# Kernel tuning notes

Measured on AMD Instinct MI355X. Metric: run time of the kernel, lower is better.

## Reference

```python
import jax, jax.numpy as jnp
import numpy as np

# near_sym_b (13,19)-tap biorthogonal level-1 DTCWT filters (Kingsbury)
H0O = np.array([-0.0017578125, 0.0, 0.022265625, -0.046875, -0.0482421875,
                0.296875, 0.5554687500, 0.296875, -0.0482421875, -0.046875,
                0.022265625, 0.0, -0.0017578125], dtype=np.float32)
H1O = np.array([-7.0626e-05, 0.0, 1.34189e-03, -1.88341e-03, -7.15660e-03,
                2.38560e-02, 5.56431e-02, -5.16881e-02, -2.99758e-01,
                5.59431e-01, -2.99758e-01, -5.16881e-02, 5.56431e-02,
                2.38560e-02, -7.15660e-03, -1.88341e-03, 1.34189e-03,
                0.0, -7.0626e-05], dtype=np.float32)

def _alt(h):
    c = (len(h) - 1) // 2
    return (h * ((-1.0) ** (np.arange(len(h)) - c))).astype(np.float32)

G0O = _alt(H1O)  # synthesis lowpass  (PR complement of H1O)
G1O = _alt(H0O)  # synthesis highpass (PR complement of H0O)

DIM, HS, WS, BATCH, NB, BS = 64, 56, 56, 32, 4, 16


def _filt(x, h, axis):
    # depthwise 1D correlation with symmetric padding; x: (B,C,H,W), axis in {2,3}
    L = len(h); p = L // 2
    pad = [(0, 0)] * 4; pad[axis] = (p, p)
    xp = jnp.pad(x, pad, mode='symmetric')
    k = jnp.asarray(h, x.dtype).reshape((1, 1, L, 1) if axis == 2 else (1, 1, 1, L))
    B, C = x.shape[:2]
    y = jax.lax.conv_general_dilated(
        xp.reshape((B * C, 1) + xp.shape[2:]), k, (1, 1), 'VALID',
        dimension_numbers=('NCHW', 'OIHW', 'NCHW'))
    return y.reshape((B, C) + y.shape[2:])


def _q2c(y):
    y = y * np.float32(1.0 / np.sqrt(2.0))
    a = y[..., 0::2, 0::2]; b = y[..., 0::2, 1::2]
    c = y[..., 1::2, 0::2]; d = y[..., 1::2, 1::2]
    return (a - d, b + c), (a + d, b - c)


def _c2q(w1r, w1i, w2r, w2i):
    sc = np.float32(1.0 / np.sqrt(2.0))
    B, C, Hh, Wh = w1r.shape
    top = jnp.stack([(w1r + w2r) * sc, (w1i + w2i) * sc], axis=-1).reshape(B, C, Hh, 2 * Wh)
    bot = jnp.stack([(w1i - w2i) * sc, (w2r - w1r) * sc], axis=-1).reshape(B, C, Hh, 2 * Wh)
    return jnp.stack([top, bot], axis=3).reshape(B, C, 2 * Hh, 2 * Wh)


def dtcwt_fwd_j1(x):
    lo = _filt(x, H0O, 3); hi = _filt(x, H1O, 3)
    ll = _filt(lo, H0O, 2)
    (d15r, d15i), (d165r, d165i) = _q2c(_filt(lo, H1O, 2))   # LH -> 15/165 deg
    (d75r, d75i), (d105r, d105i) = _q2c(_filt(hi, H0O, 2))   # HL -> 75/105 deg
    (d45r, d45i), (d135r, d135i) = _q2c(_filt(hi, H1O, 2))   # HH -> 45/135 deg
    real = jnp.stack([d15r, d45r, d75r, d105r, d135r, d165r], axis=2)
    imag = jnp.stack([d15i, d45i, d75i, d105i, d135i, d165i], axis=2)
    return ll, jnp.stack([real, imag], axis=-1)  # (B,C,H,W), (B,C,6,H/2,W/2,2)


def dtcwt_inv_j1(ll, yh):
    r = yh[..., 0]; im = yh[..., 1]
    lh = _c2q(r[:, :, 0], im[:, :, 0], r[:, :, 5], im[:, :, 5])
    hl = _c2q(r[:, :, 2], im[:, :, 2], r[:, :, 3], im[:, :, 3])
    hh = _c2q(r[:, :, 1], im[:, :, 1], r[:, :, 4], im[:, :, 4])
    lo = _filt(ll, G0O, 2) + _filt(lh, G1O, 2)
    hi = _filt(hl, G0O, 2) + _filt(hh, G1O, 2)
    return _filt(lo, G0O, 3) + _filt(hi, G1O, 3)


def setup_inputs():
    key = jax.random.key(0)
    ks = jax.random.split(key, 6)
    return {
        'x': jax.random.normal(ks[0], (BATCH, HS * WS, DIM), jnp.float32),
        'w_ll': jax.random.normal(ks[1], (DIM, HS, WS), jnp.float32) * 0.02,
        'w1': jax.random.normal(ks[2], (2, NB, BS, BS), jnp.float32) * 0.02,
        'w2': jax.random.normal(ks[3], (2, NB, BS, BS), jnp.float32) * 0.02,
        'b1': jax.random.normal(ks[4], (2, NB, BS), jnp.float32) * 0.02,
        'b2': jax.random.normal(ks[5], (2, NB, BS), jnp.float32) * 0.02,
        'H': HS, 'W': WS,
    }


def reference(x, w_ll, w1, w2, b1, b2, H, W):
    Bt, N, C = x.shape
    xi = jnp.transpose(x.reshape(Bt, H, W, C), (0, 3, 1, 2)).astype(jnp.float32)
    xl, xh = dtcwt_fwd_j1(xi)
    xl = xl * w_ll                                  # (B,C,H,W) * (C,H,W)
    Hh, Wh = H // 2, W // 2
    # (B,C,6,Hh,Wh,2) -> (2,B,6,Hh,Wh,C) -> split C into (NB,BS) blocks
    xh = jnp.transpose(xh, (5, 0, 2, 3, 4, 1)).reshape(2, Bt, 6, Hh, Wh, NB, BS)
    xr, xim = xh[0], xh[1]
    mul = lambda t, w: jnp.einsum('...bd,bdk->...bk', t, w)
    r1 = jax.nn.relu(mul(xr, w1[0]) - mul(xim, w1[1]) + b1[0])
    i1 = jax.nn.relu(mul(xr, w1[1]) + mul(xim, w1[0]) + b1[1])
    r2 = mul(r1, w2[0]) - mul(i1, w2[1]) + b2[0]
    i2 = mul(r1, w2[1]) + mul(i1, w2[0]) + b2[1]
    xh2 = jnp.stack([r2, i2], axis=-1).reshape(Bt, 6, Hh, Wh, C, 2)
    xh2 = jnp.transpose(xh2, (0, 4, 1, 2, 3, 5))    # (B,C,6,Hh,Wh,2)
    y = dtcwt_inv_j1(xl, xh2)
    return jnp.transpose(y, (0, 2, 3, 1)).reshape(Bt, N, C)
```

## Files before the change

kernel.cpp:

```cpp
#include <hip/hip_runtime.h>

#define BT 32
#define CH 64
#define HS 56
#define WS 56
#define HH 28
#define WH 28

namespace {
constexpr float ISQ2 = 0.70710678118654752440f;
constexpr float F_H0[13] = {-0.0017578125f, 0.0f, 0.022265625f, -0.046875f,
    -0.0482421875f, 0.296875f, 0.55546875f, 0.296875f, -0.0482421875f,
    -0.046875f, 0.022265625f, 0.0f, -0.0017578125f};
constexpr float F_H1[19] = {-7.0626e-05f, 0.0f, 0.00134189f, -0.00188341f,
    -0.0071566f, 0.023856f, 0.0556431f, -0.0516881f, -0.299758f, 0.559431f,
    -0.299758f, -0.0516881f, 0.0556431f, 0.023856f, -0.0071566f,
    -0.00188341f, 0.00134189f, 0.0f, -7.0626e-05f};
constexpr float F_G0[19] = {7.0626e-05f, 0.0f, -0.00134189f, -0.00188341f,
    0.0071566f, 0.023856f, -0.0556431f, -0.0516881f, 0.299758f, 0.559431f,
    0.299758f, -0.0516881f, -0.0556431f, 0.023856f, 0.0071566f,
    -0.00188341f, -0.00134189f, 0.0f, 7.0626e-05f};
constexpr float F_G1[13] = {-0.0017578125f, 0.0f, 0.022265625f, 0.046875f,
    -0.0482421875f, -0.296875f, 0.55546875f, -0.296875f, -0.0482421875f,
    0.046875f, 0.022265625f, 0.0f, -0.0017578125f};
}

__device__ __forceinline__ int symi(int k) {
    k = (k < 0) ? (-1 - k) : k;
    k = (k >= HS) ? (2 * HS - 1 - k) : k;
    return k;
}

__device__ __forceinline__ unsigned short f2bf(float f) {
    unsigned u = __float_as_uint(f);
    u += 0x7fffu + ((u >> 16) & 1u);
    return (unsigned short)(u >> 16);
}
__device__ __forceinline__ float bf2f(unsigned short h) {
    return __uint_as_float(((unsigned)h) << 16);
}
__device__ __forceinline__ float2 bfp2(unsigned u) {
    float2 r;
    r.x = __uint_as_float((u & 0xffffu) << 16);
    r.y = __uint_as_float(u & 0xffff0000u);
    return r;
}
__device__ __forceinline__ unsigned packbf(float a, float b) {
    return (unsigned)f2bf(a) | ((unsigned)f2bf(b) << 16);
}

typedef __attribute__((ext_vector_type(8))) short short8;
typedef __attribute__((ext_vector_type(4))) float f32x4;

#define PPOS 784

__global__ __launch_bounds__(256) void k_wll_T(const float* __restrict__ wll,
                                               float* __restrict__ wllT) {
    __shared__ float tile[64][65];
    int pos0 = blockIdx.x * 64;
    int lp = threadIdx.x & 63, g = threadIdx.x >> 6;
#pragma unroll
    for (int r = 0; r < 16; ++r) {
        int cc = r * 4 + g;
        tile[cc][lp] = wll[cc * (HS * WS) + pos0 + lp];
    }
    __syncthreads();
#pragma unroll
    for (int r = 0; r < 16; ++r) {
        int pl = r * 4 + g;
        wllT[(pos0 + pl) * CH + lp] = tile[lp][pl];
    }
}

__global__ __launch_bounds__(256) void k_fwd_rows(const float* __restrict__ x,
                                                  unsigned short* __restrict__ lo,
                                                  unsigned short* __restrict__ hi) {
    int b = blockIdx.x / HS, h = blockIdx.x % HS;
    int strip = threadIdx.x >> 5;
    int c0 = (threadIdx.x & 31) * 2;
    int base = (b * HS + h) * WS * CH + c0;
    const float* row = x + base;
    unsigned short* lop = lo + base;
    unsigned short* hip = hi + base;
    int w0s = strip * 7;
    float Wa[19], Wb[19];
#pragma unroll
    for (int t = 0; t < 19; ++t) {
        float2 v = *(const float2*)(row + symi(w0s - 9 + t) * CH);
        Wa[t] = v.x; Wb[t] = v.y;
    }
    float2 nW[7];
#pragma unroll
    for (int u = 0; u < 7; ++u) nW[u] = *(const float2*)(row + symi(w0s + u + 10) * CH);
#pragma unroll
    for (int u = 0; u < 7; ++u) {
        int w = w0s + u;
        float aLo = 0.f, aHi = 0.f, bLo = 0.f, bHi = 0.f;
#pragma unroll
        for (int t = 0; t < 13; ++t) { aLo += F_H0[t] * Wa[3 + t]; bLo += F_H0[t] * Wb[3 + t]; }
#pragma unroll
        for (int t = 0; t < 19; ++t) { aHi += F_H1[t] * Wa[t]; bHi += F_H1[t] * Wb[t]; }
        *(unsigned*)(lop + w * CH) = packbf(aLo, bLo);
        *(unsigned*)(hip + w * CH) = packbf(aHi, bHi);
#pragma unroll
        for (int t = 0; t < 18; ++t) { Wa[t] = Wa[t + 1]; Wb[t] = Wb[t + 1]; }
        Wa[18] = nW[u].x; Wb[18] = nW[u].y;
    }
}

__global__ __launch_bounds__(256) void k_cols_lo(
    const unsigned short* __restrict__ lo, const float* __restrict__ wllT,
    float* __restrict__ xl, unsigned short* __restrict__ sbT) {
    __shared__ float qT[4][64][15];
    int hf = blockIdx.y;
    int b = blockIdx.x / WH, wp = blockIdx.x % WH;
    int w0 = 2 * wp, tid = threadIdx.x;
    int q = tid >> 6, c = tid & 63;
    int rp = q >> 1, jc = q & 1;
    const unsigned short* colbase = lo + (b * HS) * WS * CH + (w0 + jc) * CH + c;
    {
        int hstart = 2 * (hf * 14) + rp;
        float W[19];
#pragma unroll
        for (int t = 0; t < 19; ++t) W[t] = bf2f(colbase[symi(hstart - 9 + t) * (WS * CH)]);
        for (int g = 0; g < 2; ++g) {
            float nW0[7], nW1[7], nwll[7];
            int ii0 = g * 7;
#pragma unroll
            for (int u = 0; u < 7; ++u) {
                int h = hstart + 2 * (ii0 + u);
                nW0[u] = bf2f(colbase[symi(h + 10) * (WS * CH)]);
                nW1[u] = bf2f(colbase[symi(h + 11) * (WS * CH)]);
            }
#pragma unroll
            for (int u = 0; u < 7; ++u) {
                int h = hstart + 2 * (ii0 + u);
                nwll[u] = wllT[(h * WS + (w0 + jc)) * CH + c];
            }
#pragma unroll
            for (int u = 0; u < 7; ++u) {
                int ii = ii0 + u;
                int h = hstart + 2 * ii;
                float vll = 0.f, vlh = 0.f;
#pragma unroll
                for (int t = 0; t < 13; ++t) vll += F_H0[t] * W[3 + t];
#pragma unroll
                for (int t = 0; t < 19; ++t) vlh += F_H1[t] * W[t];
                xl[((b * HS + h) * WS + (w0 + jc)) * CH + c] = vll * nwll[u];
                qT[q][c][ii] = vlh;
#pragma unroll
                for (int t = 0; t < 17; ++t) W[t] = W[t + 2];
                W[17] = nW0[u];
                W[18] = nW1[u];
            }
        }
    }
    __syncthreads();
    {
        int qq = tid >> 5;
        int role = qq & 3, half = qq >> 2;
        int c0 = (tid & 31) * 2;
        int rowA = role & 1, rowB = 3 - (role & 1);
        float sgn = (role == 1 || role == 2) ? 1.f : -1.f;
        int p = (role < 2) ? role : role + 8;
        const float* qA0 = &qT[rowA][c0][0];
        const float* qA1 = &qT[rowA][c0 + 1][0];
        const float* qB0 = &qT[rowB][c0][0];
        const float* qB1 = &qT[rowB][c0 + 1][0];
        unsigned short* dst = sbT + ((p * BT + b) * PPOS + wp * 28 + hf * 14) * CH + c0;
#pragma unroll
        for (int g = 0; g < 7; ++g) {
            int ii = half * 7 + g;
            float v0 = (qA0[ii] + sgn * qB0[ii]) * ISQ2;
            float v1 = (qA1[ii] + sgn * qB1[ii]) * ISQ2;
            *(unsigned*)(dst + ii * CH) = packbf(v0, v1);
        }
    }
}

__global__ __launch_bounds__(256) void k_cols_hi(const unsigned short* __restrict__ hi,
                                                 unsigned short* __restrict__ sbT) {
    __shared__ float qT[2][4][64][15];
    int hf = blockIdx.y;
    int b = blockIdx.x / WH, wp = blockIdx.x % WH;
    int w0 = 2 * wp, tid = threadIdx.x;
    int q = tid >> 6, c = tid & 63;
    int rp = q >> 1, jc = q & 1;
    const unsigned short* colbase = hi + (b * HS) * WS * CH + (w0 + jc) * CH + c;
    {
        int hstart = 2 * (hf * 14) + rp;
        float W[19];
#pragma unroll
        for (int t = 0; t < 19; ++t) W[t] = bf2f(colbase[symi(hstart - 9 + t) * (WS * CH)]);
        for (int g = 0; g < 2; ++g) {
            float nW0[7], nW1[7];
            int ii0 = g * 7;
#pragma unroll
            for (int u = 0; u < 7; ++u) {
                int h = hstart + 2 * (ii0 + u);
                nW0[u] = bf2f(colbase[symi(h + 10) * (WS * CH)]);
                nW1[u] = bf2f(colbase[symi(h + 11) * (WS * CH)]);
            }
#pragma unroll
            for (int u = 0; u < 7; ++u) {
                int ii = ii0 + u;
                float vhl = 0.f, vhh = 0.f;
#pragma unroll
                for (int t = 0; t < 13; ++t) vhl += F_H0[t] * W[3 + t];
#pragma unroll
                for (int t = 0; t < 19; ++t) vhh += F_H1[t] * W[t];
                qT[0][q][c][ii] = vhl;
                qT[1][q][c][ii] = vhh;
#pragma unroll
                for (int t = 0; t < 17; ++t) W[t] = W[t + 2];
                W[17] = nW0[u];
                W[18] = nW1[u];
            }
        }
    }
    __syncthreads();
    {
        int qq = tid >> 5;
        int role = qq & 3, half = qq >> 2;
        int c0 = (tid & 31) * 2;
        int rowA = role & 1, rowB = 3 - (role & 1);
        float sgn = (role == 1 || role == 2) ? 1.f : -1.f;
#pragma unroll
        for (int src = 0; src < 2; ++src) {
            int p = (src == 0) ? (4 + role) : ((role < 2) ? (2 + role) : (6 + role));
            const float* qA0 = &qT[src][rowA][c0][0];
            const float* qA1 = &qT[src][rowA][c0 + 1][0];
            const float* qB0 = &qT[src][rowB][c0][0];
            const float* qB1 = &qT[src][rowB][c0 + 1][0];
            unsigned short* dst = sbT + ((p * BT + b) * PPOS + wp * 28 + hf * 14) * CH + c0;
#pragma unroll
            for (int g = 0; g < 7; ++g) {
                int ii = half * 7 + g;
                float v0 = (qA0[ii] + sgn * qB0[ii]) * ISQ2;
                float v1 = (qA1[ii] + sgn * qB1[ii]) * ISQ2;
                *(unsigned*)(dst + ii * CH) = packbf(v0, v1);
            }
        }
    }
}

__global__ __launch_bounds__(256) void k_mix(
    const unsigned short* __restrict__ sbT, const float* __restrict__ w1,
    const float* __restrict__ w2, const float* __restrict__ b1,
    const float* __restrict__ b2, unsigned short* __restrict__ P0,
    unsigned short* __restrict__ P1, unsigned short* __restrict__ P2) {
    __shared__ unsigned short l1a[4][16][36];
    __shared__ unsigned short l1b[4][16][36];
    int blk = blockIdx.x;
    int pr = blk / (BT * 7);
    int rem = blk % (BT * 7);
    int b = rem / 7;
    int chunk = rem % 7;
    int sa = (pr == 0) ? 0 : (pr == 1) ? 2 : 1;
    int sb = (pr == 0) ? 5 : (pr == 1) ? 3 : 4;
    unsigned short* Pd = (pr == 0) ? P0 : (pr == 1) ? P1 : P2;
    int tid = threadIdx.x;
    int lane = tid & 63;
    int wv = tid >> 6;
    int nb = __builtin_amdgcn_readfirstlane(wv);
    int quad = lane >> 4;
    int n = lane & 15;

    short8 B1r, B1i, B2r, B2i;
#pragma unroll
    for (int j = 0; j < 8; ++j) {
        int kk = quad * 8 + j;
        int riw = kk >> 4, dd = kk & 15;
        float v1r = w1[nb * 256 + dd * 16 + n];
        float v1i = w1[1024 + nb * 256 + dd * 16 + n];
        float v2r = w2[nb * 256 + dd * 16 + n];
        float v2i = w2[1024 + nb * 256 + dd * 16 + n];
        B1r[j] = (short)f2bf(riw ? -v1i : v1r);
        B1i[j] = (short)f2bf(riw ? v1r : v1i);
        B2r[j] = (short)f2bf(riw ? -v2i : v2r);
        B2i[j] = (short)f2bf(riw ? v2r : v2i);
    }
    float bias1r = b1[nb * 16 + n], bias1i = b1[64 + nb * 16 + n];
    float bias2r = b2[nb * 16 + n], bias2i = b2[64 + nb * 16 + n];

    int rix = quad >> 1, dlo = (quad & 1) * 8;
    const unsigned short* pAa =
        sbT + (((sa * 2 + rix) * BT + b) * PPOS + n) * CH + nb * 16 + dlo;
    const unsigned short* pAb =
        sbT + (((sb * 2 + rix) * BT + b) * PPOS + n) * CH + nb * 16 + dlo;

    int pbase = chunk * 112;
    for (int t = 0; t < 7; ++t) {
        int pos0 = pbase + t * 16;
        short8 A1a = *(const short8*)(pAa + pos0 * CH);
        short8 A1b = *(const short8*)(pAb + pos0 * CH);
        f32x4 a1r = {bias1r, bias1r, bias1r, bias1r};
        f32x4 a1i = {bias1i, bias1i, bias1i, bias1i};
        f32x4 b1r_ = a1r, b1i_ = a1i;
        a1r = __builtin_amdgcn_mfma_f32_16x16x32_bf16(A1a, B1r, a1r, 0, 0, 0);
        a1i = __builtin_amdgcn_mfma_f32_16x16x32_bf16(A1a, B1i, a1i, 0, 0, 0);
        b1r_ = __builtin_amdgcn_mfma_f32_16x16x32_bf16(A1b, B1r, b1r_, 0, 0, 0);
        b1i_ = __builtin_amdgcn_mfma_f32_16x16x32_bf16(A1b, B1i, b1i_, 0, 0, 0);
#pragma unroll
        for (int r = 0; r < 4; ++r) {
            int pos = quad * 4 + r;
            l1a[wv][pos][n] = f2bf(fmaxf(a1r[r], 0.f));
            l1a[wv][pos][16 + n] = f2bf(fmaxf(a1i[r], 0.f));
            l1b[wv][pos][n] = f2bf(fmaxf(b1r_[r], 0.f));
            l1b[wv][pos][16 + n] = f2bf(fmaxf(b1i_[r], 0.f));
        }
        union { short8 s8; uint2 u2[2]; } a2a, a2b;
        const unsigned short* rowpa = &l1a[wv][n][0];
        const unsigned short* rowpb = &l1b[wv][n][0];
        a2a.u2[0] = *(const uint2*)(rowpa + quad * 8);
        a2a.u2[1] = *(const uint2*)(rowpa + quad * 8 + 4);
        a2b.u2[0] = *(const uint2*)(rowpb + quad * 8);
        a2b.u2[1] = *(const uint2*)(rowpb + quad * 8 + 4);
        f32x4 aAr = {bias2r, bias2r, bias2r, bias2r};
        f32x4 aAi = {bias2i, bias2i, bias2i, bias2i};
        f32x4 aBr = aAr, aBi = aAi;
        aAr = __builtin_amdgcn_mfma_f32_16x16x32_bf16(a2a.s8, B2r, aAr, 0, 0, 0);
        aAi = __builtin_amdgcn_mfma_f32_16x16x32_bf16(a2a.s8, B2i, aAi, 0, 0, 0);
        aBr = __builtin_amdgcn_mfma_f32_16x16x32_bf16(a2b.s8, B2r, aBr, 0, 0, 0);
        aBi = __builtin_amdgcn_mfma_f32_16x16x32_bf16(a2b.s8, B2i, aBi, 0, 0, 0);
#pragma unroll
        for (int r = 0; r < 4; ++r) {
            int pos_g = pos0 + quad * 4 + r;
            int wp = pos_g / 28, ii = pos_g - wp * 28;
            int o = ((b * HS + 2 * ii) * WS + 2 * wp) * CH + nb * 16 + n;
            Pd[o] = f2bf((aAr[r] + aBr[r]) * ISQ2);
            Pd[o + CH] = f2bf((aAi[r] + aBi[r]) * ISQ2);
            Pd[o + WS * CH] = f2bf((aAi[r] - aBi[r]) * ISQ2);
            Pd[o + WS * CH + CH] = f2bf((aBr[r] - aAr[r]) * ISQ2);
        }
    }
}

template <int MODE>
__device__ __forceinline__ void inv_cols_body(
    const float* __restrict__ xl, const unsigned short* __restrict__ P0,
    const unsigned short* __restrict__ P1, const unsigned short* __restrict__ P2,
    float* __restrict__ lo2, float* __restrict__ hi2) {
    int hf = blockIdx.y;
    int b = blockIdx.x / 7, wg = blockIdx.x % 7;
    int wl = threadIdx.x >> 5, l = threadIdx.x & 31;
    int c0 = l * 2;
    int w = wg * 8 + wl;
    int base = (b * HS) * WS * CH + w * CH + c0;
    const int st = WS * CH;
    const unsigned short* Bp = (MODE == 0) ? P0 : P2;
    float* outp = (MODE == 0) ? lo2 : hi2;
    auto ldA = [&](int r) -> float2 {
        if (MODE == 0) return *(const float2*)(xl + base + r * st);
        return bfp2(*(const unsigned*)(P1 + base + r * st));
    };
    auto ldB = [&](int r) -> float2 {
        return bfp2(*(const unsigned*)(Bp + base + r * st));
    };
    int h0 = hf * 28;
    float Aa[19], Ab[19], Ba[13], Bb[13];
#pragma unroll
    for (int t = 0; t < 19; ++t) { float2 v = ldA(symi(h0 - 9 + t)); Aa[t] = v.x; Ab[t] = v.y; }
#pragma unroll
    for (int t = 0; t < 13; ++t) { float2 v = ldB(symi(h0 - 6 + t)); Ba[t] = v.x; Bb[t] = v.y; }
    for (int g = 0; g < 7; ++g) {
        float2 nA[4], nB[4];
        int hg = h0 + g * 4;
#pragma unroll
        for (int u = 0; u < 4; ++u) nA[u] = ldA(symi(hg + u + 10));
#pragma unroll
        for (int u = 0; u < 4; ++u) nB[u] = ldB(symi(hg + u + 7));
#pragma unroll
        for (int u = 0; u < 4; ++u) {
            int h = hg + u;
            float acca = 0.f, accb = 0.f;
#pragma unroll
            for (int t = 0; t < 19; ++t) { acca += F_G0[t] * Aa[t]; accb += F_G0[t] * Ab[t]; }
#pragma unroll
            for (int t = 0; t < 13; ++t) { acca += F_G1[t] * Ba[t]; accb += F_G1[t] * Bb[t]; }
            float2 ov; ov.x = acca; ov.y = accb;
            *(float2*)(outp + base + h * st) = ov;
#pragma unroll
            for (int t = 0; t < 18; ++t) { Aa[t] = Aa[t + 1]; Ab[t] = Ab[t + 1]; }
#pragma unroll
            for (int t = 0; t < 12; ++t) { Ba[t] = Ba[t + 1]; Bb[t] = Bb[t + 1]; }
            Aa[18] = nA[u].x; Ab[18] = nA[u].y;
            Ba[12] = nB[u].x; Bb[12] = nB[u].y;
        }
    }
}

__global__ __launch_bounds__(256) void k_inv_cols(
    const float* __restrict__ xl, const unsigned short* __restrict__ P0,
    const unsigned short* __restrict__ P1, const unsigned short* __restrict__ P2,
    float* __restrict__ lo2, float* __restrict__ hi2) {
    if (blockIdx.z == 0)
        inv_cols_body<0>(xl, P0, P1, P2, lo2, hi2);
    else
        inv_cols_body<1>(xl, P0, P1, P2, lo2, hi2);
}

__global__ __launch_bounds__(256) void k_inv_rows(const float* __restrict__ lo2,
                                                  const float* __restrict__ hi2,
                                                  float* __restrict__ out) {
    int b = blockIdx.x / HS, h = blockIdx.x % HS;
    int strip = threadIdx.x >> 5;
    int c0 = (threadIdx.x & 31) * 2;
    int base = (b * HS + h) * WS * CH + c0;
    const float* rlo = lo2 + base;
    const float* rhi = hi2 + base;
    float* op = out + base;
    int w0s = strip * 7;
    float Aa[19], Ab[19], Ba[13], Bb[13];
#pragma unroll
    for (int t = 0; t < 19; ++t) {
        float2 v = *(const float2*)(rlo + symi(w0s - 9 + t) * CH);
        Aa[t] = v.x; Ab[t] = v.y;
    }
#pragma unroll
    for (int t = 0; t < 13; ++t) {
        float2 v = *(const float2*)(rhi + symi(w0s - 6 + t) * CH);
        Ba[t] = v.x; Bb[t] = v.y;
    }
    float2 nA[7], nB[7];
#pragma unroll
    for (int u = 0; u < 7; ++u) nA[u] = *(const float2*)(rlo + symi(w0s + u + 10) * CH);
#pragma unroll
    for (int u = 0; u < 7; ++u) nB[u] = *(const float2*)(rhi + symi(w0s + u + 7) * CH);
#pragma unroll
    for (int u = 0; u < 7; ++u) {
        int w = w0s + u;
        float acca = 0.f, accb = 0.f;
#pragma unroll
        for (int t = 0; t < 19; ++t) { acca += F_G0[t] * Aa[t]; accb += F_G0[t] * Ab[t]; }
#pragma unroll
        for (int t = 0; t < 13; ++t) { acca += F_G1[t] * Ba[t]; accb += F_G1[t] * Bb[t]; }
        float2 ov; ov.x = acca; ov.y = accb;
        *(float2*)(op + w * CH) = ov;
#pragma unroll
        for (int t = 0; t < 18; ++t) { Aa[t] = Aa[t + 1]; Ab[t] = Ab[t + 1]; }
#pragma unroll
        for (int t = 0; t < 12; ++t) { Ba[t] = Ba[t + 1]; Bb[t] = Bb[t + 1]; }
        Aa[18] = nA[u].x; Ab[18] = nA[u].y;
        Ba[12] = nB[u].x; Bb[12] = nB[u].y;
    }
}

extern "C" void kernel_launch(void* const* d_in, const int* in_sizes, int n_in,
                              void* d_out, int out_size, void* d_ws, size_t ws_size,
                              hipStream_t stream) {
    const float* x = (const float*)d_in[0];
    const float* w_ll = (const float*)d_in[1];
    const float* w1 = (const float*)d_in[2];
    const float* w2 = (const float*)d_in[3];
    const float* b1 = (const float*)d_in[4];
    const float* b2 = (const float*)d_in[5];
    float* out = (float*)d_out;

    const size_t A = (size_t)BT * HS * WS * CH;
    const size_t SBf = (size_t)12 * 64 * BT * PPOS / 2;
    float* wsf = (float*)d_ws;
    float* xl = wsf;
    unsigned short* sbT = (unsigned short*)(wsf + A);
    float* lo2 = wsf + A;
    float* hi2 = wsf + A + SBf;
    unsigned short* lo_in = (unsigned short*)(wsf + A + SBf + A);
    unsigned short* hi_in = lo_in + A;
    unsigned short* P0 = hi_in + A;
    unsigned short* P1 = P0 + A;
    unsigned short* P2 = P1 + A;

    float* wllT = out;

    k_wll_T<<<49, 256, 0, stream>>>(w_ll, wllT);
    k_fwd_rows<<<BT * HS, 256, 0, stream>>>(x, lo_in, hi_in);
    k_cols_lo<<<dim3(BT * WH, 2), 256, 0, stream>>>(lo_in, wllT, xl, sbT);
    k_cols_hi<<<dim3(BT * WH, 2), 256, 0, stream>>>(hi_in, sbT);
    k_mix<<<3 * BT * 7, 256, 0, stream>>>(sbT, w1, w2, b1, b2, P0, P1, P2);
    k_inv_cols<<<dim3(BT * 7, 2, 2), 256, 0, stream>>>(xl, P0, P1, P2, lo2, hi2);
    k_inv_rows<<<BT * HS, 256, 0, stream>>>(lo2, hi2, out);
}
```

Measured before the change: 180.1 us.

## Merge forward column kernels and split column/mix kernels into finer grids

Merges the lo and hi forward column kernels into one launch that uses a z-dimension to pick the source, and halves the rows each block handles (7 instead of 14) so the grid has more blocks. The mix kernel moves from 4 waves per block to one 64-thread block per channel group with a grid y dimension, and prefetches the next A tile in a register double buffer. The inverse column kernel also splits its height into quarters. The aim is more parallelism and one fewer launch, in exchange for more halo reloading of the filter window per block.

```diff
diff --git a/kernel.cpp b/kernel.cpp
--- a/kernel.cpp
+++ b/kernel.cpp
@@ -108,161 +108,106 @@
     }
 }
 
-__global__ __launch_bounds__(256) void k_cols_lo(
-    const unsigned short* __restrict__ lo, const float* __restrict__ wllT,
+__global__ __launch_bounds__(256) void k_cols(
+    const unsigned short* __restrict__ lo_in,
+    const unsigned short* __restrict__ hi_in, const float* __restrict__ wllT,
     float* __restrict__ xl, unsigned short* __restrict__ sbT) {
-    __shared__ float qT[4][64][15];
-    int hf = blockIdx.y;
+    __shared__ float qT[2][4][64][9];
+    int hq = blockIdx.y;
+    int zmode = blockIdx.z;
     int b = blockIdx.x / WH, wp = blockIdx.x % WH;
     int w0 = 2 * wp, tid = threadIdx.x;
     int q = tid >> 6, c = tid & 63;
     int rp = q >> 1, jc = q & 1;
-    const unsigned short* colbase = lo + (b * HS) * WS * CH + (w0 + jc) * CH + c;
+    const unsigned short* srcp = zmode ? hi_in : lo_in;
+    const unsigned short* colbase = srcp + (b * HS) * WS * CH + (w0 + jc) * CH + c;
     {
-        int hstart = 2 * (hf * 14) + rp;
+        int hstart = 14 * hq + rp;
         float W[19];
 #pragma unroll
         for (int t = 0; t < 19; ++t) W[t] = bf2f(colbase[symi(hstart - 9 + t) * (WS * CH)]);
-        for (int g = 0; g < 2; ++g) {
-            float nW0[7], nW1[7], nwll[7];
-            int ii0 = g * 7;
-#pragma unroll
-            for (int u = 0; u < 7; ++u) {
-                int h = hstart + 2 * (ii0 + u);
-                nW0[u] = bf2f(colbase[symi(h + 10) * (WS * CH)]);
-                nW1[u] = bf2f(colbase[symi(h + 11) * (WS * CH)]);
+        float nW0[7], nW1[7], nwll[7];
+#pragma unroll
+        for (int u = 0; u < 7; ++u) {
+            int h = hstart + 2 * u;
+            nW0[u] = bf2f(colbase[symi(h + 10) * (WS * CH)]);
+            nW1[u] = bf2f(colbase[symi(h + 11) * (WS * CH)]);
+        }
+        if (zmode == 0) {
+#pragma unroll
+            for (int u = 0; u < 7; ++u)
+                nwll[u] = wllT[((hstart + 2 * u) * WS + (w0 + jc)) * CH + c];
+        }
+#pragma unroll
+        for (int u = 0; u < 7; ++u) {
+            int h = hstart + 2 * u;
+            float v0 = 0.f, v1 = 0.f;
+#pragma unroll
+            for (int t = 0; t < 13; ++t) v0 += F_H0[t] * W[3 + t];
+#pragma unroll
+            for (int t = 0; t < 19; ++t) v1 += F_H1[t] * W[t];
+            if (zmode == 0) {
+                xl[((b * HS + h) * WS + (w0 + jc)) * CH + c] = v0 * nwll[u];
+                qT[0][q][c][u] = v1;
+            } else {
+                qT[0][q][c][u] = v0;
+                qT[1][q][c][u] = v1;
             }
 #pragma unroll
-            for (int u = 0; u < 7; ++u) {
-                int h = hstart + 2 * (ii0 + u);
-                nwll[u] = wllT[(h * WS + (w0 + jc)) * CH + c];
-            }
-#pragma unroll
-            for (int u = 0; u < 7; ++u) {
-                int ii = ii0 + u;
-                int h = hstart + 2 * ii;
-                float vll = 0.f, vlh = 0.f;
-#pragma unroll
-                for (int t = 0; t < 13; ++t) vll += F_H0[t] * W[3 + t];
-#pragma unroll
-                for (int t = 0; t < 19; ++t) vlh += F_H1[t] * W[t];
-                xl[((b * HS + h) * WS + (w0 + jc)) * CH + c] = vll * nwll[u];
-                qT[q][c][ii] = vlh;
-#pragma unroll
-                for (int t = 0; t < 17; ++t) W[t] = W[t + 2];
-                W[17] = nW0[u];
-                W[18] = nW1[u];
-            }
+            for (int t = 0; t < 17; ++t) W[t] = W[t + 2];
+            W[17] = nW0[u];
+            W[18] = nW1[u];
         }
     }
     __syncthreads();
     {
         int qq = tid >> 5;
-        int role = qq & 3, half = qq >> 2;
+        int role = qq & 3, sub = qq >> 2;
         int c0 = (tid & 31) * 2;
         int rowA = role & 1, rowB = 3 - (role & 1);
         float sgn = (role == 1 || role == 2) ? 1.f : -1.f;
-        int p = (role < 2) ? role : role + 8;
-        const float* qA0 = &qT[rowA][c0][0];
-        const float* qA1 = &qT[rowA][c0 + 1][0];
-        const float* qB0 = &qT[rowB][c0][0];
-        const float* qB1 = &qT[rowB][c0 + 1][0];
-        unsigned short* dst = sbT + ((p * BT + b) * PPOS + wp * 28 + hf * 14) * CH + c0;
-#pragma unroll
-        for (int g = 0; g < 7; ++g) {
-            int ii = half * 7 + g;
-            float v0 = (qA0[ii] + sgn * qB0[ii]) * ISQ2;
-            float v1 = (qA1[ii] + sgn * qB1[ii]) * ISQ2;
-            *(unsigned*)(dst + ii * CH) = packbf(v0, v1);
-        }
-    }
-}
-
-__global__ __launch_bounds__(256) void k_cols_hi(const unsigned short* __restrict__ hi,
-                                                 unsigned short* __restrict__ sbT) {
-    __shared__ float qT[2][4][64][15];
-    int hf = blockIdx.y;
-    int b = blockIdx.x / WH, wp = blockIdx.x % WH;
-    int w0 = 2 * wp, tid = threadIdx.x;
-    int q = tid >> 6, c = tid & 63;
-    int rp = q >> 1, jc = q & 1;
-    const unsigned short* colbase = hi + (b * HS) * WS * CH + (w0 + jc) * CH + c;
-    {
-        int hstart = 2 * (hf * 14) + rp;
-        float W[19];
-#pragma unroll
-        for (int t = 0; t < 19; ++t) W[t] = bf2f(colbase[symi(hstart - 9 + t) * (WS * CH)]);
-        for (int g = 0; g < 2; ++g) {
-            float nW0[7], nW1[7];
-            int ii0 = g * 7;
-#pragma unroll
-            for (int u = 0; u < 7; ++u) {
-                int h = hstart + 2 * (ii0 + u);
-                nW0[u] = bf2f(colbase[symi(h + 10) * (WS * CH)]);
-                nW1[u] = bf2f(colbase[symi(h + 11) * (WS * CH)]);
-            }
-#pragma unroll
-            for (int u = 0; u < 7; ++u) {
-                int ii = ii0 + u;
-                float vhl = 0.f, vhh = 0.f;
-#pragma unroll
-                for (int t = 0; t < 13; ++t) vhl += F_H0[t] * W[3 + t];
-#pragma unroll
-                for (int t = 0; t < 19; ++t) vhh += F_H1[t] * W[t];
-                qT[0][q][c][ii] = vhl;
-                qT[1][q][c][ii] = vhh;
-#pragma unroll
-                for (int t = 0; t < 17; ++t) W[t] = W[t + 2];
-                W[17] = nW0[u];
-                W[18] = nW1[u];
-            }
-        }
-    }
-    __syncthreads();
-    {
-        int qq = tid >> 5;
-        int role = qq & 3, half = qq >> 2;
-        int c0 = (tid & 31) * 2;
-        int rowA = role & 1, rowB = 3 - (role & 1);
-        float sgn = (role == 1 || role == 2) ? 1.f : -1.f;
-#pragma unroll
-        for (int src = 0; src < 2; ++src) {
-            int p = (src == 0) ? (4 + role) : ((role < 2) ? (2 + role) : (6 + role));
-            const float* qA0 = &qT[src][rowA][c0][0];
-            const float* qA1 = &qT[src][rowA][c0 + 1][0];
-            const float* qB0 = &qT[src][rowB][c0][0];
-            const float* qB1 = &qT[src][rowB][c0 + 1][0];
-            unsigned short* dst = sbT + ((p * BT + b) * PPOS + wp * 28 + hf * 14) * CH + c0;
-#pragma unroll
-            for (int g = 0; g < 7; ++g) {
-                int ii = half * 7 + g;
-                float v0 = (qA0[ii] + sgn * qB0[ii]) * ISQ2;
-                float v1 = (qA1[ii] + sgn * qB1[ii]) * ISQ2;
+        int iL = sub * 4, iH = sub ? 7 : 4;
+        int posb = wp * 28 + hq * 7;
+        if (zmode == 0) {
+            int p = (role < 2) ? role : role + 8;
+            unsigned short* dst = sbT + ((p * BT + b) * PPOS + posb) * CH + c0;
+            for (int ii = iL; ii < iH; ++ii) {
+                float v0 = (qT[0][rowA][c0][ii] + sgn * qT[0][rowB][c0][ii]) * ISQ2;
+                float v1 = (qT[0][rowA][c0 + 1][ii] + sgn * qT[0][rowB][c0 + 1][ii]) * ISQ2;
                 *(unsigned*)(dst + ii * CH) = packbf(v0, v1);
             }
-        }
-    }
-}
-
-__global__ __launch_bounds__(256) void k_mix(
+        } else {
+#pragma unroll
+            for (int src = 0; src < 2; ++src) {
+                int p = (src == 0) ? (4 + role) : ((role < 2) ? (2 + role) : (6 + role));
+                unsigned short* dst = sbT + ((p * BT + b) * PPOS + posb) * CH + c0;
+                for (int ii = iL; ii < iH; ++ii) {
+                    float v0 = (qT[src][rowA][c0][ii] + sgn * qT[src][rowB][c0][ii]) * ISQ2;
+                    float v1 = (qT[src][rowA][c0 + 1][ii] + sgn * qT[src][rowB][c0 + 1][ii]) * ISQ2;
+                    *(unsigned*)(dst + ii * CH) = packbf(v0, v1);
+                }
+            }
+        }
+    }
+}
+
+__global__ __launch_bounds__(64) void k_mix(
     const unsigned short* __restrict__ sbT, const float* __restrict__ w1,
     const float* __restrict__ w2, const float* __restrict__ b1,
     const float* __restrict__ b2, unsigned short* __restrict__ P0,
     unsigned short* __restrict__ P1, unsigned short* __restrict__ P2) {
-    __shared__ unsigned short l1a[4][16][36];
-    __shared__ unsigned short l1b[4][16][36];
+    __shared__ unsigned short l1a[16][36];
+    __shared__ unsigned short l1b[16][36];
     int blk = blockIdx.x;
     int pr = blk / (BT * 7);
     int rem = blk % (BT * 7);
     int b = rem / 7;
     int chunk = rem % 7;
+    int nb = blockIdx.y;
     int sa = (pr == 0) ? 0 : (pr == 1) ? 2 : 1;
     int sb = (pr == 0) ? 5 : (pr == 1) ? 3 : 4;
     unsigned short* Pd = (pr == 0) ? P0 : (pr == 1) ? P1 : P2;
-    int tid = threadIdx.x;
-    int lane = tid & 63;
-    int wv = tid >> 6;
-    int nb = __builtin_amdgcn_readfirstlane(wv);
+    int lane = threadIdx.x;
     int quad = lane >> 4;
     int n = lane & 15;
 
@@ -290,10 +235,15 @@
         sbT + (((sb * 2 + rix) * BT + b) * PPOS + n) * CH + nb * 16 + dlo;
 
     int pbase = chunk * 112;
+    short8 A1a = *(const short8*)(pAa + pbase * CH);
+    short8 A1b = *(const short8*)(pAb + pbase * CH);
     for (int t = 0; t < 7; ++t) {
         int pos0 = pbase + t * 16;
-        short8 A1a = *(const short8*)(pAa + pos0 * CH);
-        short8 A1b = *(const short8*)(pAb + pos0 * CH);
+        short8 nAa = A1a, nAb = A1b;
+        if (t < 6) {
+            nAa = *(const short8*)(pAa + (pos0 + 16) * CH);
+            nAb = *(const short8*)(pAb + (pos0 + 16) * CH);
+        }
         f32x4 a1r = {bias1r, bias1r, bias1r, bias1r};
         f32x4 a1i = {bias1i, bias1i, bias1i, bias1i};
         f32x4 b1r_ = a1r, b1i_ = a1i;
@@ -304,14 +254,14 @@
 #pragma unroll
         for (int r = 0; r < 4; ++r) {
             int pos = quad * 4 + r;
-            l1a[wv][pos][n] = f2bf(fmaxf(a1r[r], 0.f));
-            l1a[wv][pos][16 + n] = f2bf(fmaxf(a1i[r], 0.f));
-            l1b[wv][pos][n] = f2bf(fmaxf(b1r_[r], 0.f));
-            l1b[wv][pos][16 + n] = f2bf(fmaxf(b1i_[r], 0.f));
+            l1a[pos][n] = f2bf(fmaxf(a1r[r], 0.f));
+            l1a[pos][16 + n] = f2bf(fmaxf(a1i[r], 0.f));
+            l1b[pos][n] = f2bf(fmaxf(b1r_[r], 0.f));
+            l1b[pos][16 + n] = f2bf(fmaxf(b1i_[r], 0.f));
         }
         union { short8 s8; uint2 u2[2]; } a2a, a2b;
-        const unsigned short* rowpa = &l1a[wv][n][0];
-        const unsigned short* rowpb = &l1b[wv][n][0];
+        const unsigned short* rowpa = &l1a[n][0];
+        const unsigned short* rowpb = &l1b[n][0];
         a2a.u2[0] = *(const uint2*)(rowpa + quad * 8);
         a2a.u2[1] = *(const uint2*)(rowpa + quad * 8 + 4);
         a2b.u2[0] = *(const uint2*)(rowpb + quad * 8);
@@ -333,6 +283,7 @@
             Pd[o + WS * CH] = f2bf((aAi[r] - aBi[r]) * ISQ2);
             Pd[o + WS * CH + CH] = f2bf((aBr[r] - aAr[r]) * ISQ2);
         }
+        A1a = nAa; A1b = nAb;
     }
 }
 
@@ -357,21 +308,23 @@
     auto ldB = [&](int r) -> float2 {
         return bfp2(*(const unsigned*)(Bp + base + r * st));
     };
-    int h0 = hf * 28;
+    int h0 = hf * 14;
     float Aa[19], Ab[19], Ba[13], Bb[13];
 #pragma unroll
     for (int t = 0; t < 19; ++t) { float2 v = ldA(symi(h0 - 9 + t)); Aa[t] = v.x; Ab[t] = v.y; }
 #pragma unroll
     for (int t = 0; t < 13; ++t) { float2 v = ldB(symi(h0 - 6 + t)); Ba[t] = v.x; Bb[t] = v.y; }
-    for (int g = 0; g < 7; ++g) {
+    int hg = h0;
+#pragma unroll
+    for (int g = 0; g < 4; ++g) {
+        const int cnt = (g < 3) ? 4 : 2;
         float2 nA[4], nB[4];
-        int hg = h0 + g * 4;
-#pragma unroll
-        for (int u = 0; u < 4; ++u) nA[u] = ldA(symi(hg + u + 10));
-#pragma unroll
-        for (int u = 0; u < 4; ++u) nB[u] = ldB(symi(hg + u + 7));
-#pragma unroll
-        for (int u = 0; u < 4; ++u) {
+#pragma unroll
+        for (int u = 0; u < cnt; ++u) nA[u] = ldA(symi(hg + u + 10));
+#pragma unroll
+        for (int u = 0; u < cnt; ++u) nB[u] = ldB(symi(hg + u + 7));
+#pragma unroll
+        for (int u = 0; u < cnt; ++u) {
             int h = hg + u;
             float acca = 0.f, accb = 0.f;
 #pragma unroll
@@ -387,6 +340,7 @@
             Aa[18] = nA[u].x; Ab[18] = nA[u].y;
             Ba[12] = nB[u].x; Bb[12] = nB[u].y;
         }
+        hg += cnt;
     }
 }
 
@@ -474,9 +428,8 @@
 
     k_wll_T<<<49, 256, 0, stream>>>(w_ll, wllT);
     k_fwd_rows<<<BT * HS, 256, 0, stream>>>(x, lo_in, hi_in);
-    k_cols_lo<<<dim3(BT * WH, 2), 256, 0, stream>>>(lo_in, wllT, xl, sbT);
-    k_cols_hi<<<dim3(BT * WH, 2), 256, 0, stream>>>(hi_in, sbT);
-    k_mix<<<3 * BT * 7, 256, 0, stream>>>(sbT, w1, w2, b1, b2, P0, P1, P2);
-    k_inv_cols<<<dim3(BT * 7, 2, 2), 256, 0, stream>>>(xl, P0, P1, P2, lo2, hi2);
+    k_cols<<<dim3(BT * WH, 4, 2), 256, 0, stream>>>(lo_in, hi_in, wllT, xl, sbT);
+    k_mix<<<dim3(3 * BT * 7, 4), 64, 0, stream>>>(sbT, w1, w2, b1, b2, P0, P1, P2);
+    k_inv_cols<<<dim3(BT * 7, 4, 2), 256, 0, stream>>>(xl, P0, P1, P2, lo2, hi2);
     k_inv_rows<<<BT * HS, 256, 0, stream>>>(lo2, hi2, out);
 }
```

After: 182.9 us. No clear change (+1.5%).
